# Performance work log

Hardware: AMD Instinct MI355X
Metric: run time of the kernel (lower is better)

## Reference

```python
import jax, jax.numpy as jnp
import numpy as np

B, S, H = 2, 2048, 2048
NH, NKV, HD = 16, 4, 128
THETA = 10000.0


def _rope_cos_sin(seq_len, head_dim, theta, dtype):
    inv_freq = 1.0 / (theta ** (jnp.arange(0, head_dim, 2, dtype=jnp.float32) / head_dim))
    t = jnp.arange(seq_len, dtype=jnp.float32)
    freqs = t[:, None] * inv_freq[None, :]          # [S, HD/2]
    emb = jnp.concatenate([freqs, freqs], axis=-1)  # [S, HD]
    return jnp.cos(emb).astype(dtype), jnp.sin(emb).astype(dtype)


def _rotate_half(x):
    d = x.shape[-1] // 2
    return jnp.concatenate([-x[..., d:], x[..., :d]], axis=-1)


def setup_inputs() -> dict:
    key = jax.random.key(0)
    ks = jax.random.split(key, 5)
    x = jax.random.normal(ks[0], (B, S, H), dtype=jnp.float32)
    Wq = jax.random.normal(ks[1], (NH * HD, H), dtype=jnp.float32) * 0.02
    Wk = jax.random.normal(ks[2], (NKV * HD, H), dtype=jnp.float32) * 0.02
    Wv = jax.random.normal(ks[3], (NKV * HD, H), dtype=jnp.float32) * 0.02
    Wo = jax.random.normal(ks[4], (H, H), dtype=jnp.float32) * 0.02
    causal = jnp.tril(jnp.ones((S, S), dtype=bool))
    attention_mask = jnp.where(causal, 0.0, -1e9).astype(jnp.float32)[None, None]  # [1,1,S,S]
    return {"x": x, "attention_mask": attention_mask, "Wq": Wq, "Wk": Wk, "Wv": Wv, "Wo": Wo}


def reference(x, attention_mask, Wq, Wk, Wv, Wo):
    b, s, _ = x.shape
    q = (x @ Wq.T).reshape(b, s, NH, HD).transpose(0, 2, 1, 3)    # [b,nh,s,hd]
    k = (x @ Wk.T).reshape(b, s, NKV, HD).transpose(0, 2, 1, 3)   # [b,nkv,s,hd]
    v = (x @ Wv.T).reshape(b, s, NKV, HD).transpose(0, 2, 1, 3)
    cos, sin = _rope_cos_sin(s, HD, THETA, x.dtype)               # [s,hd] each
    cos = cos[None, None]; sin = sin[None, None]
    q = q * cos + _rotate_half(q) * sin
    k = k * cos + _rotate_half(k) * sin
    rep = NH // NKV
    k = jnp.repeat(k, rep, axis=1)                                 # [b,nh,s,hd]
    v = jnp.repeat(v, rep, axis=1)
    scores = jnp.einsum('bhqd,bhkd->bhqk', q, k) / jnp.sqrt(jnp.asarray(HD, x.dtype))
    scores = scores + attention_mask
    attn = jax.nn.softmax(scores, axis=-1)
    out = jnp.einsum('bhqk,bhkd->bhqd', attn, v)                   # [b,nh,s,hd]
    out = out.transpose(0, 2, 1, 3).reshape(b, s, NH * HD)
    return out @ Wo.T
```

## Files before the change

kernel.cpp:

```cpp
#include <hip/hip_runtime.h>

typedef unsigned short u16;
typedef __bf16 bf16x8 __attribute__((ext_vector_type(8)));
typedef float f32x4 __attribute__((ext_vector_type(4)));

#define S_LEN  2048
#define NHEADS 16
#define NKVH   4
#define HDIM   128
#define BB     2
#define MROWS  4096
#define QKV_N  3072
#define HID    2048

__device__ __forceinline__ u16 f2b(float f) {
  union { float f; unsigned u; } x; x.f = f;
  unsigned r = x.u + 0x7fffu + ((x.u >> 16) & 1u);
  return (u16)(r >> 16);
}
__device__ __forceinline__ u16 f2b_fast(float f) {
  union { float f; unsigned u; } x; x.f = f;
  return (u16)((x.u + 0x8000u) >> 16);
}
__device__ __forceinline__ float b2f(u16 v) {
  union { unsigned u; float f; } x; x.u = ((unsigned)v) << 16;
  return x.f;
}
__device__ __forceinline__ void gload_lds16(const u16* g, u16* l) {
  __builtin_amdgcn_global_load_lds((__attribute__((address_space(1))) void*)g,
                                   (__attribute__((address_space(3))) void*)l,
                                   16, 0, 0);
}

__global__ void k_f2b4(const float* __restrict__ in, u16* __restrict__ out, int n4) {
  int i = blockIdx.x * blockDim.x + threadIdx.x;
  if (i >= n4) return;
  float4 v = ((const float4*)in)[i];
  ushort4 o;
  o.x = f2b(v.x); o.y = f2b(v.y); o.z = f2b(v.z); o.w = f2b(v.w);
  ((ushort4*)out)[i] = o;
}

__global__ void k_cs(float* __restrict__ cs) {
  int s = blockIdx.x, j = threadIdx.x;
  float inv = expf(-(float)j * 0.14391156831212787f);
  float ang = (float)s * inv;
  float c, sn;
  sincosf(ang, &sn, &c);
  cs[(s * 64 + j) * 2 + 0] = c;
  cs[(s * 64 + j) * 2 + 1] = sn;
}

template <int OUT_BF16>
__global__ __launch_bounds__(256) void k_gemm_bt(
    const u16* __restrict__ A, const u16* __restrict__ Bm, void* __restrict__ Cv,
    int M, int N, int K)
{
  __shared__ u16 Al[128 * 32];
  __shared__ u16 Bl[128 * 32];
  const int tid = threadIdx.x;
  const int wave = tid >> 6, lane = tid & 63;
  const int l15 = lane & 15, l4 = lane >> 4;
  const int wr = wave >> 1, wc = wave & 1;
  const int row0 = blockIdx.y * 128, col0 = blockIdx.x * 128;

  f32x4 zero = {0.f, 0.f, 0.f, 0.f};
  f32x4 acc[4][4];
#pragma unroll
  for (int m = 0; m < 4; ++m)
#pragma unroll
    for (int n = 0; n < 4; ++n) acc[m][n] = zero;

  const int e0 = lane * 8;
  for (int kb = 0; kb < K; kb += 32) {
#pragma unroll
    for (int it = 0; it < 2; ++it) {
      const int chunk = it * 4 + wave;
      const int e = chunk * 512 + e0;
      const int r = e >> 5, c = e & 31;
      gload_lds16(A + (size_t)(row0 + r) * K + kb + c, Al + chunk * 512);
      gload_lds16(Bm + (size_t)(col0 + r) * K + kb + c, Bl + chunk * 512);
    }
    __syncthreads();
    bf16x8 af[4], bfv[4];
#pragma unroll
    for (int m = 0; m < 4; ++m)
      af[m] = *(const bf16x8*)(Al + (wr * 64 + m * 16 + l15) * 32 + l4 * 8);
#pragma unroll
    for (int n = 0; n < 4; ++n)
      bfv[n] = *(const bf16x8*)(Bl + (wc * 64 + n * 16 + l15) * 32 + l4 * 8);
#pragma unroll
    for (int m = 0; m < 4; ++m)
#pragma unroll
      for (int n = 0; n < 4; ++n)
        acc[m][n] = __builtin_amdgcn_mfma_f32_16x16x32_bf16(af[m], bfv[n], acc[m][n], 0, 0, 0);
    __syncthreads();
  }
#pragma unroll
  for (int m = 0; m < 4; ++m) {
    const int r = row0 + wr * 64 + m * 16 + l4 * 4;
#pragma unroll
    for (int n = 0; n < 4; ++n) {
      const int c = col0 + wc * 64 + n * 16 + l15;
#pragma unroll
      for (int j = 0; j < 4; ++j) {
        const float v = acc[m][n][j];
        if (OUT_BF16) ((u16*)Cv)[(size_t)(r + j) * N + c] = f2b(v);
        else          ((float*)Cv)[(size_t)(r + j) * N + c] = v;
      }
    }
  }
}

__global__ __launch_bounds__(256) void k_rope(
    const u16* __restrict__ qkv, const float* __restrict__ cs,
    u16* __restrict__ Qr, u16* __restrict__ Kr)
{
  const int row = blockIdx.x;
  const int b = row >> 11, s = row & 2047;
  const int t = threadIdx.x;
  const u16* src = qkv + (size_t)row * QKV_N;
#pragma unroll
  for (int p = t; p < 1024; p += 256) {
    const int h = p >> 6, j = p & 63;
    const float c = cs[(s * 64 + j) * 2], sn = cs[(s * 64 + j) * 2 + 1];
    const float x0 = b2f(src[h * 128 + j]);
    const float x1 = b2f(src[h * 128 + 64 + j]);
    const size_t base = ((size_t)(b * NHEADS + h) * S_LEN + s) * HDIM;
    Qr[base + j]      = f2b(x0 * c - x1 * sn);
    Qr[base + 64 + j] = f2b(x1 * c + x0 * sn);
  }
  {
    const int h = t >> 6, j = t & 63;
    const float c = cs[(s * 64 + j) * 2], sn = cs[(s * 64 + j) * 2 + 1];
    const float x0 = b2f(src[2048 + h * 128 + j]);
    const float x1 = b2f(src[2048 + h * 128 + 64 + j]);
    const size_t base = ((size_t)(b * NKVH + h) * S_LEN + s) * HDIM;
    Kr[base + j]      = f2b(x0 * c - x1 * sn);
    Kr[base + 64 + j] = f2b(x1 * c + x0 * sn);
  }
}

__global__ __launch_bounds__(256) void k_vtrans(
    const u16* __restrict__ qkv, u16* __restrict__ Vt)
{
  const int blk = blockIdx.x;
  const int b = blk >> 7, s0 = (blk & 127) << 4;
  const int tid = threadIdx.x;
#pragma unroll
  for (int vi = 0; vi < 2; ++vi) {
    const int idx = vi * 256 + tid;
    const int h = idx >> 7, d = idx & 127;
    union { u16 u[16]; uint4 v[2]; } bb;
#pragma unroll
    for (int s = 0; s < 16; ++s)
      bb.u[s] = qkv[(size_t)(b * S_LEN + s0 + s) * QKV_N + 2560 + idx];
    u16* dst = Vt + ((size_t)(b * NKVH + h) * HDIM + d) * S_LEN + s0;
    *(uint4*)(dst)     = bb.v[0];
    *(uint4*)(dst + 8) = bb.v[1];
  }
}

__device__ __forceinline__ void attn_qtile(
    int qt, int lastPhase,
    const u16* __restrict__ Q, const u16* __restrict__ Kg, const u16* __restrict__ Vg,
    u16* __restrict__ Out, int bh,
    u16* Kl0, u16* Kl1, u16* Vl0, u16* Vl1, char* Pb,
    const int (&ko)[2], const int (&vo)[2],
    int wave, int lane, int& cur)
{
  const int l15 = lane & 15, l4 = lane >> 4;
  const int b = bh >> 4, h = bh & 15;
  const int qw0 = qt * 128 + wave * 16;
  const u16* Qg = Q + ((size_t)bh * S_LEN + qw0) * HDIM;

  bf16x8 qf[4];
#pragma unroll
  for (int kc = 0; kc < 4; ++kc)
    qf[kc] = *(const bf16x8*)(Qg + l15 * HDIM + kc * 32 + l4 * 8);

  f32x4 zero = {0.f, 0.f, 0.f, 0.f};
  f32x4 oacc[8];
#pragma unroll
  for (int i = 0; i < 8; ++i) oacc[i] = zero;
  float m_r[4], l_p[4];
#pragma unroll
  for (int j = 0; j < 4; ++j) { m_r[j] = -1e30f; l_p[j] = 0.f; }

  const float S2 = 0.08838834764831845f * 1.4426950408889634f;
  const int nt = 2 * (qt + 1);

  for (int t = 0; t < nt; ++t) {
    const int kt = t * 64;
    u16* Vb = cur ? Vl1 : Vl0;
#pragma unroll
    for (int it = 0; it < 2; ++it)
      gload_lds16(Vg + (size_t)vo[it] + kt, Vb + (it * 8 + wave) * 512);
    const int hasNext = (t + 1 < nt) || (!lastPhase);
    const int ktn = (t + 1 < nt) ? kt + 64 : 0;
    u16* Kn = cur ? Kl0 : Kl1;
    if (hasNext) {
#pragma unroll
      for (int it = 0; it < 2; ++it)
        gload_lds16(Kg + (size_t)ktn * HDIM + ko[it], Kn + (it * 8 + wave) * 512);
      asm volatile("s_waitcnt vmcnt(4)" ::: "memory");
    } else {
      asm volatile("s_waitcnt vmcnt(2)" ::: "memory");
    }
    __builtin_amdgcn_sched_barrier(0);
    __builtin_amdgcn_s_barrier();
    __builtin_amdgcn_sched_barrier(0);

    const char* Kb = (const char*)(cur ? Kl1 : Kl0);
    const int act = (kt <= qw0 + 15);
    if (act) {
      f32x4 s[4];
#pragma unroll
      for (int n = 0; n < 4; ++n) s[n] = zero;
      __builtin_amdgcn_s_setprio(1);
#pragma unroll
      for (int n = 0; n < 4; ++n) {
        const int row = n * 16 + l15;
#pragma unroll
        for (int kc = 0; kc < 4; ++kc) {
          const int ab = (row * 256 + kc * 64 + l4 * 16) ^ ((row & 7) << 4);
          bf16x8 kf = *(const bf16x8*)(Kb + ab);
          s[n] = __builtin_amdgcn_mfma_f32_16x16x32_bf16(qf[kc], kf, s[n], 0, 0, 0);
        }
      }
      __builtin_amdgcn_s_setprio(0);
      float sv[4][4], pm[4];
      if (kt + 63 > qw0) {
#pragma unroll
        for (int j = 0; j < 4; ++j) {
          const int qg = qw0 + l4 * 4 + j;
#pragma unroll
          for (int n = 0; n < 4; ++n) {
            float x = s[n][j] * S2;
            if (kt + n * 16 + l15 > qg) x = -1e30f;
            sv[n][j] = x;
          }
        }
      } else {
#pragma unroll
        for (int j = 0; j < 4; ++j)
#pragma unroll
          for (int n = 0; n < 4; ++n) sv[n][j] = s[n][j] * S2;
      }
#pragma unroll
      for (int j = 0; j < 4; ++j)
        pm[j] = fmaxf(fmaxf(sv[0][j], sv[1][j]), fmaxf(sv[2][j], sv[3][j]));
      bool ok = true;
#pragma unroll
      for (int j = 0; j < 4; ++j) ok = ok && (pm[j] <= m_r[j] + 11.5416f);
      if (!__all(ok)) {
#pragma unroll
        for (int off = 1; off < 16; off <<= 1)
#pragma unroll
          for (int j = 0; j < 4; ++j)
            pm[j] = fmaxf(pm[j], __shfl_xor(pm[j], off, 64));
        float sc[4];
#pragma unroll
        for (int j = 0; j < 4; ++j) {
          const float mn = fmaxf(m_r[j], pm[j]);
          sc[j] = exp2f(m_r[j] - mn);
          m_r[j] = mn;
          l_p[j] *= sc[j];
        }
#pragma unroll
        for (int nd = 0; nd < 8; ++nd)
#pragma unroll
          for (int j = 0; j < 4; ++j) oacc[nd][j] *= sc[j];
      }
#pragma unroll
      for (int n = 0; n < 4; ++n)
#pragma unroll
        for (int j = 0; j < 4; ++j) {
          const float p = exp2f(sv[n][j] - m_r[j]);
          l_p[j] += p;
          const int prow = l4 * 4 + j;
          const int pb = (prow * 128 + (n * 16 + l15) * 2) ^ ((prow & 7) << 4);
          *(u16*)(Pb + pb) = f2b_fast(p);
        }
    }
    if (hasNext) asm volatile("s_waitcnt vmcnt(2)" ::: "memory");
    else         asm volatile("s_waitcnt vmcnt(0)" ::: "memory");
    __builtin_amdgcn_sched_barrier(0);
    __builtin_amdgcn_s_barrier();
    __builtin_amdgcn_sched_barrier(0);
    if (act) {
      __builtin_amdgcn_s_setprio(1);
#pragma unroll
      for (int kc2 = 0; kc2 < 2; ++kc2) {
        const int prow = l15;
        const int pbo = (prow * 128 + kc2 * 64 + l4 * 16) ^ ((prow & 7) << 4);
        bf16x8 pf = *(const bf16x8*)(Pb + pbo);
#pragma unroll
        for (int nd = 0; nd < 8; ++nd) {
          const int d = nd * 16 + l15;
          const int ab = (d * 128 + kc2 * 64 + l4 * 16) ^ ((d & 7) << 4);
          bf16x8 vf = *(const bf16x8*)((const char*)Vb + ab);
          oacc[nd] = __builtin_amdgcn_mfma_f32_16x16x32_bf16(pf, vf, oacc[nd], 0, 0, 0);
        }
      }
      __builtin_amdgcn_s_setprio(0);
    }
    cur ^= 1;
  }

#pragma unroll
  for (int off = 1; off < 16; off <<= 1)
#pragma unroll
    for (int j = 0; j < 4; ++j)
      l_p[j] += __shfl_xor(l_p[j], off, 64);
  float il[4];
#pragma unroll
  for (int j = 0; j < 4; ++j) il[j] = 1.f / l_p[j];
  const size_t obase = ((size_t)b * S_LEN + qw0 + l4 * 4) * HID + h * HDIM;
#pragma unroll
  for (int nd = 0; nd < 8; ++nd)
#pragma unroll
    for (int j = 0; j < 4; ++j)
      Out[obase + (size_t)j * HID + nd * 16 + l15] = f2b(oacc[nd][j] * il[j]);
}

__global__ __launch_bounds__(512) void k_attn(
    const u16* __restrict__ Q, const u16* __restrict__ Kr,
    const u16* __restrict__ Vt, u16* __restrict__ Out)
{
  __shared__ u16 Kl[2][64 * 128];
  __shared__ u16 Vl[2][128 * 64];
  __shared__ u16 Pl[8][16 * 64];
  const int tid = threadIdx.x;
  const int wave = tid >> 6, lane = tid & 63;
  const int bh = blockIdx.x;
  const int pairi = blockIdx.y;
  const int b = bh >> 4, h = bh & 15;
  const int kvh = h >> 2;

  const u16* Kg = Kr + (size_t)(b * NKVH + kvh) * S_LEN * HDIM;
  const u16* Vg = Vt + (size_t)(b * NKVH + kvh) * HDIM * S_LEN;

  int ko[2], vo[2];
#pragma unroll
  for (int it = 0; it < 2; ++it) {
    const int c = it * 8 + wave;
    const int L = c * 1024 + lane * 16;
    const int r = L >> 8;  const int w2 = (L & 255) ^ ((r & 7) << 4);
    ko[it] = r * HDIM + (w2 >> 1);
    const int d = L >> 7;  const int wv = (L & 127) ^ ((d & 7) << 4);
    vo[it] = d * S_LEN + (wv >> 1);
  }
#pragma unroll
  for (int it = 0; it < 2; ++it)
    gload_lds16(Kg + ko[it], &Kl[0][(it * 8 + wave) * 512]);

  char* Pb = (char*)&Pl[wave][0];
  int cur = 0;
  attn_qtile(15 - pairi, 0, Q, Kg, Vg, Out, bh, &Kl[0][0], &Kl[1][0],
             &Vl[0][0], &Vl[1][0], Pb, ko, vo, wave, lane, cur);
  attn_qtile(pairi,      1, Q, Kg, Vg, Out, bh, &Kl[0][0], &Kl[1][0],
             &Vl[0][0], &Vl[1][0], Pb, ko, vo, wave, lane, cur);
}

extern "C" void kernel_launch(void* const* d_in, const int* in_sizes, int n_in,
                              void* d_out, int out_size, void* d_ws, size_t ws_size,
                              hipStream_t stream)
{
  const float* x  = (const float*)d_in[0];
  const float* Wq = (const float*)d_in[2];
  const float* Wk = (const float*)d_in[3];
  const float* Wv = (const float*)d_in[4];
  const float* Wo = (const float*)d_in[5];
  float* out = (float*)d_out;

  u16* xb    = (u16*)d_ws;
  u16* Wqkvb = xb    + (size_t)MROWS * HID;
  u16* Wob   = Wqkvb + (size_t)QKV_N * HID;
  u16* qkv   = Wob   + (size_t)HID * HID;
  u16* Qr    = qkv   + (size_t)MROWS * QKV_N;
  u16* Kr    = Qr    + (size_t)BB * NHEADS * S_LEN * HDIM;
  u16* Vt    = Kr    + (size_t)BB * NKVH * S_LEN * HDIM;
  u16* attn  = Vt    + (size_t)BB * NKVH * S_LEN * HDIM;
  float* cs  = (float*)(attn + (size_t)MROWS * HID);

  k_f2b4<<<dim3((MROWS * HID / 4) / 256), 256, 0, stream>>>(x, xb, MROWS * HID / 4);
  k_f2b4<<<dim3((HID * HID / 4) / 256), 256, 0, stream>>>(Wq, Wqkvb, HID * HID / 4);
  k_f2b4<<<dim3((512 * HID / 4) / 256), 256, 0, stream>>>(Wk, Wqkvb + (size_t)2048 * HID, 512 * HID / 4);
  k_f2b4<<<dim3((512 * HID / 4) / 256), 256, 0, stream>>>(Wv, Wqkvb + (size_t)2560 * HID, 512 * HID / 4);
  k_f2b4<<<dim3((HID * HID / 4) / 256), 256, 0, stream>>>(Wo, Wob, HID * HID / 4);
  k_cs<<<dim3(S_LEN), dim3(64), 0, stream>>>(cs);
  k_gemm_bt<1><<<dim3(QKV_N / 128, MROWS / 128), 256, 0, stream>>>(xb, Wqkvb, qkv, MROWS, QKV_N, HID);
  k_rope<<<dim3(MROWS), 256, 0, stream>>>(qkv, cs, Qr, Kr);
  k_vtrans<<<dim3(BB * 128), 256, 0, stream>>>(qkv, Vt);
  k_attn<<<dim3(BB * NHEADS, 8), 512, 0, stream>>>(Qr, Kr, Vt, attn);
  k_gemm_bt<0><<<dim3(HID / 128, MROWS / 128), 256, 0, stream>>>(attn, Wob, out, MROWS, HID, HID);
}
```

Baseline: 237.3 us.

## Fuse prep kernels, fold softmax scale into Q, shrink attention tiles to 64 rows

Merges the five float-to-bf16 conversion launches and the cos/sin table kernel into one prep kernel. It also fuses RoPE with the V transpose and folds the softmax scale into Q at RoPE time. The attention kernel moves from 128-row query tiles with 8 waves to 64-row tiles with 4 waves and a doubled grid, and the per-wave causal activity check is removed. This cuts launch overhead and the per-score multiply and gives more blocks for load balance, at the cost of less K/V reuse per block and an extra bf16 rounding of the pre-scaled Q.

Result: no change. 235.4 us (-0.8%).

```diff
diff --git a/kernel.cpp b/kernel.cpp
--- a/kernel.cpp
+++ b/kernel.cpp
@@ -32,23 +32,38 @@
                                    16, 0, 0);
 }
 
-__global__ void k_f2b4(const float* __restrict__ in, u16* __restrict__ out, int n4) {
-  int i = blockIdx.x * blockDim.x + threadIdx.x;
-  if (i >= n4) return;
-  float4 v = ((const float4*)in)[i];
+#define PB_X   8192
+#define PB_WQ  (PB_X + 4096)
+#define PB_WK  (PB_WQ + 1024)
+#define PB_WV  (PB_WK + 1024)
+#define PB_WO  (PB_WV + 4096)
+#define PB_CS  (PB_WO + 512)
+__global__ void k_prep(const float* __restrict__ x,
+                       const float* __restrict__ Wq, const float* __restrict__ Wk,
+                       const float* __restrict__ Wv, const float* __restrict__ Wo,
+                       u16* __restrict__ xb, u16* __restrict__ Wqkvb,
+                       u16* __restrict__ Wob, float* __restrict__ cs)
+{
+  const int bid = blockIdx.x, tid = threadIdx.x;
+  const float* src; u16* dst; int i;
+  if (bid < PB_X)       { i = bid * 256 + tid;            src = x;  dst = xb; }
+  else if (bid < PB_WQ) { i = (bid - PB_X) * 256 + tid;   src = Wq; dst = Wqkvb; }
+  else if (bid < PB_WK) { i = (bid - PB_WQ) * 256 + tid;  src = Wk; dst = Wqkvb + (size_t)2048 * HID; }
+  else if (bid < PB_WV) { i = (bid - PB_WK) * 256 + tid;  src = Wv; dst = Wqkvb + (size_t)2560 * HID; }
+  else if (bid < PB_WO) { i = (bid - PB_WV) * 256 + tid;  src = Wo; dst = Wob; }
+  else {
+    const int p = (bid - PB_WO) * 256 + tid;
+    const int s = p >> 6, j = p & 63;
+    float inv = expf(-(float)j * 0.14391156831212787f);
+    float ang = (float)s * inv;
+    float c, sn; sincosf(ang, &sn, &c);
+    cs[p * 2 + 0] = c; cs[p * 2 + 1] = sn;
+    return;
+  }
+  float4 v = ((const float4*)src)[i];
   ushort4 o;
   o.x = f2b(v.x); o.y = f2b(v.y); o.z = f2b(v.z); o.w = f2b(v.w);
-  ((ushort4*)out)[i] = o;
-}
-
-__global__ void k_cs(float* __restrict__ cs) {
-  int s = blockIdx.x, j = threadIdx.x;
-  float inv = expf(-(float)j * 0.14391156831212787f);
-  float ang = (float)s * inv;
-  float c, sn;
-  sincosf(ang, &sn, &c);
-  cs[(s * 64 + j) * 2 + 0] = c;
-  cs[(s * 64 + j) * 2 + 1] = sn;
+  ((ushort4*)dst)[i] = o;
 }
 
 template <int OUT_BF16>
@@ -112,52 +127,44 @@
   }
 }
 
-__global__ __launch_bounds__(256) void k_rope(
+__global__ __launch_bounds__(256) void k_ropev(
     const u16* __restrict__ qkv, const float* __restrict__ cs,
-    u16* __restrict__ Qr, u16* __restrict__ Kr)
-{
-  const int row = blockIdx.x;
-  const int b = row >> 11, s = row & 2047;
-  const int t = threadIdx.x;
-  const u16* src = qkv + (size_t)row * QKV_N;
-#pragma unroll
-  for (int p = t; p < 1024; p += 256) {
-    const int h = p >> 6, j = p & 63;
-    const float c = cs[(s * 64 + j) * 2], sn = cs[(s * 64 + j) * 2 + 1];
-    const float x0 = b2f(src[h * 128 + j]);
-    const float x1 = b2f(src[h * 128 + 64 + j]);
-    const size_t base = ((size_t)(b * NHEADS + h) * S_LEN + s) * HDIM;
-    Qr[base + j]      = f2b(x0 * c - x1 * sn);
-    Qr[base + 64 + j] = f2b(x1 * c + x0 * sn);
-  }
-  {
-    const int h = t >> 6, j = t & 63;
-    const float c = cs[(s * 64 + j) * 2], sn = cs[(s * 64 + j) * 2 + 1];
-    const float x0 = b2f(src[2048 + h * 128 + j]);
-    const float x1 = b2f(src[2048 + h * 128 + 64 + j]);
-    const size_t base = ((size_t)(b * NKVH + h) * S_LEN + s) * HDIM;
+    u16* __restrict__ Qr, u16* __restrict__ Kr, u16* __restrict__ Vt)
+{
+  const int blk = blockIdx.x;
+  const int b = blk >> 8, s0 = (blk & 255) << 3;
+  const int tid = threadIdx.x;
+  const float S2 = 0.08838834764831845f * 1.4426950408889634f;
+#pragma unroll
+  for (int p = tid; p < 8192; p += 256) {
+    const int s = p >> 10, rem = p & 1023, h = rem >> 6, j = rem & 63;
+    const int sg = s0 + s;
+    const float c = cs[(sg * 64 + j) * 2], sn = cs[(sg * 64 + j) * 2 + 1];
+    const u16* src = qkv + (size_t)(b * S_LEN + sg) * QKV_N + h * 128;
+    const float x0 = b2f(src[j]), x1 = b2f(src[64 + j]);
+    const size_t base = ((size_t)(b * NHEADS + h) * S_LEN + sg) * HDIM;
+    Qr[base + j]      = f2b((x0 * c - x1 * sn) * S2);
+    Qr[base + 64 + j] = f2b((x1 * c + x0 * sn) * S2);
+  }
+#pragma unroll
+  for (int p = tid; p < 2048; p += 256) {
+    const int s = p >> 8, rem = p & 255, h = rem >> 6, j = rem & 63;
+    const int sg = s0 + s;
+    const float c = cs[(sg * 64 + j) * 2], sn = cs[(sg * 64 + j) * 2 + 1];
+    const u16* src = qkv + (size_t)(b * S_LEN + sg) * QKV_N + 2048 + h * 128;
+    const float x0 = b2f(src[j]), x1 = b2f(src[64 + j]);
+    const size_t base = ((size_t)(b * NKVH + h) * S_LEN + sg) * HDIM;
     Kr[base + j]      = f2b(x0 * c - x1 * sn);
     Kr[base + 64 + j] = f2b(x1 * c + x0 * sn);
   }
-}
-
-__global__ __launch_bounds__(256) void k_vtrans(
-    const u16* __restrict__ qkv, u16* __restrict__ Vt)
-{
-  const int blk = blockIdx.x;
-  const int b = blk >> 7, s0 = (blk & 127) << 4;
-  const int tid = threadIdx.x;
 #pragma unroll
   for (int vi = 0; vi < 2; ++vi) {
-    const int idx = vi * 256 + tid;
-    const int h = idx >> 7, d = idx & 127;
-    union { u16 u[16]; uint4 v[2]; } bb;
-#pragma unroll
-    for (int s = 0; s < 16; ++s)
+    const int idx = vi * 256 + tid, h = idx >> 7, d = idx & 127;
+    union { u16 u[8]; uint4 v; } bb;
+#pragma unroll
+    for (int s = 0; s < 8; ++s)
       bb.u[s] = qkv[(size_t)(b * S_LEN + s0 + s) * QKV_N + 2560 + idx];
-    u16* dst = Vt + ((size_t)(b * NKVH + h) * HDIM + d) * S_LEN + s0;
-    *(uint4*)(dst)     = bb.v[0];
-    *(uint4*)(dst + 8) = bb.v[1];
+    *(uint4*)(Vt + ((size_t)(b * NKVH + h) * HDIM + d) * S_LEN + s0) = bb.v;
   }
 }
 
@@ -166,12 +173,12 @@
     const u16* __restrict__ Q, const u16* __restrict__ Kg, const u16* __restrict__ Vg,
     u16* __restrict__ Out, int bh,
     u16* Kl0, u16* Kl1, u16* Vl0, u16* Vl1, char* Pb,
-    const int (&ko)[2], const int (&vo)[2],
+    const int (&ko)[4], const int (&vo)[4],
     int wave, int lane, int& cur)
 {
   const int l15 = lane & 15, l4 = lane >> 4;
   const int b = bh >> 4, h = bh & 15;
-  const int qw0 = qt * 128 + wave * 16;
+  const int qw0 = qt * 64 + wave * 16;
   const u16* Qg = Q + ((size_t)bh * S_LEN + qw0) * HDIM;
 
   bf16x8 qf[4];
@@ -187,33 +194,31 @@
 #pragma unroll
   for (int j = 0; j < 4; ++j) { m_r[j] = -1e30f; l_p[j] = 0.f; }
 
-  const float S2 = 0.08838834764831845f * 1.4426950408889634f;
-  const int nt = 2 * (qt + 1);
+  const int nt = qt + 1;
 
   for (int t = 0; t < nt; ++t) {
     const int kt = t * 64;
     u16* Vb = cur ? Vl1 : Vl0;
 #pragma unroll
-    for (int it = 0; it < 2; ++it)
-      gload_lds16(Vg + (size_t)vo[it] + kt, Vb + (it * 8 + wave) * 512);
+    for (int it = 0; it < 4; ++it)
+      gload_lds16(Vg + (size_t)vo[it] + kt, Vb + (it * 4 + wave) * 512);
     const int hasNext = (t + 1 < nt) || (!lastPhase);
     const int ktn = (t + 1 < nt) ? kt + 64 : 0;
     u16* Kn = cur ? Kl0 : Kl1;
     if (hasNext) {
 #pragma unroll
-      for (int it = 0; it < 2; ++it)
-        gload_lds16(Kg + (size_t)ktn * HDIM + ko[it], Kn + (it * 8 + wave) * 512);
+      for (int it = 0; it < 4; ++it)
+        gload_lds16(Kg + (size_t)ktn * HDIM + ko[it], Kn + (it * 4 + wave) * 512);
+      asm volatile("s_waitcnt vmcnt(8)" ::: "memory");
+    } else {
       asm volatile("s_waitcnt vmcnt(4)" ::: "memory");
-    } else {
-      asm volatile("s_waitcnt vmcnt(2)" ::: "memory");
     }
     __builtin_amdgcn_sched_barrier(0);
     __builtin_amdgcn_s_barrier();
     __builtin_amdgcn_sched_barrier(0);
 
     const char* Kb = (const char*)(cur ? Kl1 : Kl0);
-    const int act = (kt <= qw0 + 15);
-    if (act) {
+    {
       f32x4 s[4];
 #pragma unroll
       for (int n = 0; n < 4; ++n) s[n] = zero;
@@ -236,7 +241,7 @@
           const int qg = qw0 + l4 * 4 + j;
 #pragma unroll
           for (int n = 0; n < 4; ++n) {
-            float x = s[n][j] * S2;
+            float x = s[n][j];
             if (kt + n * 16 + l15 > qg) x = -1e30f;
             sv[n][j] = x;
           }
@@ -245,7 +250,7 @@
 #pragma unroll
         for (int j = 0; j < 4; ++j)
 #pragma unroll
-          for (int n = 0; n < 4; ++n) sv[n][j] = s[n][j] * S2;
+          for (int n = 0; n < 4; ++n) sv[n][j] = s[n][j];
       }
 #pragma unroll
       for (int j = 0; j < 4; ++j)
@@ -283,12 +288,12 @@
           *(u16*)(Pb + pb) = f2b_fast(p);
         }
     }
-    if (hasNext) asm volatile("s_waitcnt vmcnt(2)" ::: "memory");
+    if (hasNext) asm volatile("s_waitcnt vmcnt(4)" ::: "memory");
     else         asm volatile("s_waitcnt vmcnt(0)" ::: "memory");
     __builtin_amdgcn_sched_barrier(0);
     __builtin_amdgcn_s_barrier();
     __builtin_amdgcn_sched_barrier(0);
-    if (act) {
+    {
       __builtin_amdgcn_s_setprio(1);
 #pragma unroll
       for (int kc2 = 0; kc2 < 2; ++kc2) {
@@ -324,13 +329,13 @@
       Out[obase + (size_t)j * HID + nd * 16 + l15] = f2b(oacc[nd][j] * il[j]);
 }
 
-__global__ __launch_bounds__(512) void k_attn(
+__global__ __launch_bounds__(256) void k_attn(
     const u16* __restrict__ Q, const u16* __restrict__ Kr,
     const u16* __restrict__ Vt, u16* __restrict__ Out)
 {
   __shared__ u16 Kl[2][64 * 128];
   __shared__ u16 Vl[2][128 * 64];
-  __shared__ u16 Pl[8][16 * 64];
+  __shared__ u16 Pl[4][16 * 64];
   const int tid = threadIdx.x;
   const int wave = tid >> 6, lane = tid & 63;
   const int bh = blockIdx.x;
@@ -341,10 +346,10 @@
   const u16* Kg = Kr + (size_t)(b * NKVH + kvh) * S_LEN * HDIM;
   const u16* Vg = Vt + (size_t)(b * NKVH + kvh) * HDIM * S_LEN;
 
-  int ko[2], vo[2];
-#pragma unroll
-  for (int it = 0; it < 2; ++it) {
-    const int c = it * 8 + wave;
+  int ko[4], vo[4];
+#pragma unroll
+  for (int it = 0; it < 4; ++it) {
+    const int c = it * 4 + wave;
     const int L = c * 1024 + lane * 16;
     const int r = L >> 8;  const int w2 = (L & 255) ^ ((r & 7) << 4);
     ko[it] = r * HDIM + (w2 >> 1);
@@ -352,12 +357,12 @@
     vo[it] = d * S_LEN + (wv >> 1);
   }
 #pragma unroll
-  for (int it = 0; it < 2; ++it)
-    gload_lds16(Kg + ko[it], &Kl[0][(it * 8 + wave) * 512]);
+  for (int it = 0; it < 4; ++it)
+    gload_lds16(Kg + ko[it], &Kl[0][(it * 4 + wave) * 512]);
 
   char* Pb = (char*)&Pl[wave][0];
   int cur = 0;
-  attn_qtile(15 - pairi, 0, Q, Kg, Vg, Out, bh, &Kl[0][0], &Kl[1][0],
+  attn_qtile(31 - pairi, 0, Q, Kg, Vg, Out, bh, &Kl[0][0], &Kl[1][0],
              &Vl[0][0], &Vl[1][0], Pb, ko, vo, wave, lane, cur);
   attn_qtile(pairi,      1, Q, Kg, Vg, Out, bh, &Kl[0][0], &Kl[1][0],
              &Vl[0][0], &Vl[1][0], Pb, ko, vo, wave, lane, cur);
@@ -384,15 +389,9 @@
   u16* attn  = Vt    + (size_t)BB * NKVH * S_LEN * HDIM;
   float* cs  = (float*)(attn + (size_t)MROWS * HID);
 
-  k_f2b4<<<dim3((MROWS * HID / 4) / 256), 256, 0, stream>>>(x, xb, MROWS * HID / 4);
-  k_f2b4<<<dim3((HID * HID / 4) / 256), 256, 0, stream>>>(Wq, Wqkvb, HID * HID / 4);
-  k_f2b4<<<dim3((512 * HID / 4) / 256), 256, 0, stream>>>(Wk, Wqkvb + (size_t)2048 * HID, 512 * HID / 4);
-  k_f2b4<<<dim3((512 * HID / 4) / 256), 256, 0, stream>>>(Wv, Wqkvb + (size_t)2560 * HID, 512 * HID / 4);
-  k_f2b4<<<dim3((HID * HID / 4) / 256), 256, 0, stream>>>(Wo, Wob, HID * HID / 4);
-  k_cs<<<dim3(S_LEN), dim3(64), 0, stream>>>(cs);
+  k_prep<<<dim3(PB_CS), 256, 0, stream>>>(x, Wq, Wk, Wv, Wo, xb, Wqkvb, Wob, cs);
   k_gemm_bt<1><<<dim3(QKV_N / 128, MROWS / 128), 256, 0, stream>>>(xb, Wqkvb, qkv, MROWS, QKV_N, HID);
-  k_rope<<<dim3(MROWS), 256, 0, stream>>>(qkv, cs, Qr, Kr);
-  k_vtrans<<<dim3(BB * 128), 256, 0, stream>>>(qkv, Vt);
-  k_attn<<<dim3(BB * NHEADS, 8), 512, 0, stream>>>(Qr, Kr, Vt, attn);
+  k_ropev<<<dim3(BB * 256), 256, 0, stream>>>(qkv, cs, Qr, Kr, Vt);
+  k_attn<<<dim3(BB * NHEADS, 16), 256, 0, stream>>>(Qr, Kr, Vt, attn);
   k_gemm_bt<0><<<dim3(HID / 128, MROWS / 128), 256, 0, stream>>>(attn, Wob, out, MROWS, HID, HID);
 }
```
